# Optimization experiments

Measured on AMD Instinct MI355X. Metric: run time of the kernel, lower is better.

Reference implementation:

```python
import jax, jax.numpy as jnp
import numpy as np

K = 32        # neighbors kept
SCALE = 1     # dilation stride for dilated kNN


def setup_inputs() -> dict:
    key = jax.random.key(0)
    ks = jax.random.split(key, 8)
    s = 0.05  # weight init scale
    return {
        "x": jax.random.normal(ks[0], (16, 3, 4096), jnp.float32),
        "w1": jax.random.normal(ks[1], (64, 3), jnp.float32) * s,
        "b1": jnp.zeros((64,), jnp.float32),
        "w2": jax.random.normal(ks[2], (128, 64), jnp.float32) * s,
        "b2": jnp.zeros((128,), jnp.float32),
        "w3": jax.random.normal(ks[3], (1024, 128), jnp.float32) * s,
        "b3": jnp.zeros((1024,), jnp.float32),
        "fw1": jax.random.normal(ks[4], (512, 1024), jnp.float32) * s,
        "fb1": jnp.zeros((512,), jnp.float32),
        "fw2": jax.random.normal(ks[5], (256, 512), jnp.float32) * s,
        "fb2": jnp.zeros((256,), jnp.float32),
        "fw3": jax.random.normal(ks[6], (9, 256), jnp.float32) * s,
        "fb3": jnp.zeros((9,), jnp.float32),
    }


def _knn_idx(x):
    # x: (B, C, N). Returns (B, N, K) indices of K nearest neighbors (dilated by SCALE).
    inner = jnp.einsum('bcn,bcm->bnm', x, x)            # (B, N, N)
    sq = jnp.sum(x * x, axis=1)                          # (B, N)
    neg_dist = 2.0 * inner - sq[:, :, None] - sq[:, None, :]  # = -||xi-xj||^2
    _, idx = jax.lax.top_k(neg_dist, K * SCALE)          # (B, N, K*SCALE)
    return idx[:, :, ::SCALE]                            # (B, N, K)


def reference(x, w1, b1, w2, b2, w3, b3, fw1, fb1, fw2, fb2, fw3, fb3):
    B, C, N = x.shape
    idx = _knn_idx(x)                                    # (B, N, K)
    xt = jnp.swapaxes(x, 1, 2)                           # (B, N, C)
    # gather neighbors: nbrs[b,n,k,c] = xt[b, idx[b,n,k], c]
    nbrs = jax.vmap(lambda xb, ib: xb[ib])(xt, idx)      # (B, N, K, C)
    x0 = nbrs - xt[:, :, None, :]                        # edge features x_j - x_i

    # STN (T-Net): shared MLP over edges, global max pool, FC head -> 3x3 transform
    h = jax.nn.relu(jnp.einsum('bnkc,oc->bnko', x0, w1) + b1)
    h = jax.nn.relu(jnp.einsum('bnkc,oc->bnko', h, w2) + b2)
    h = jax.nn.relu(jnp.einsum('bnkc,oc->bnko', h, w3) + b3)
    g = jnp.max(h, axis=(1, 2))                          # (B, 1024)
    f = jax.nn.relu(g @ fw1.T + fb1)
    f = jax.nn.relu(f @ fw2.T + fb2)
    t = (f @ fw3.T + fb3).reshape(B, 3, 3) + jnp.eye(3, dtype=x.dtype)

    out = jnp.einsum('bnc,bcd->bnd', xt, t)              # bmm(x^T, t)
    return jnp.swapaxes(out, 1, 2)                       # (B, 3, N)
```

## Files before the change

kernel.cpp:

```cpp
#include <hip/hip_runtime.h>
#include <hip/hip_fp8.h>

typedef __bf16 bf16_t;
typedef __bf16 bf16x8 __attribute__((ext_vector_type(8)));
typedef float floatx16 __attribute__((ext_vector_type(16)));
typedef int intx8 __attribute__((ext_vector_type(8)));
typedef unsigned long long u64;

#define B_ 16
#define N_ 4096
#define K_ 32


__device__ __forceinline__ unsigned enc_f(float f) {
    unsigned u = __float_as_uint(f);
    return (u & 0x80000000u) ? ~u : (u | 0x80000000u);
}
__device__ __forceinline__ float dec_f(unsigned e) {
    return __uint_as_float((e & 0x80000000u) ? (e & 0x7fffffffu) : ~e);
}

__device__ __forceinline__ float max3f(float a, float b, float c) {
    float d;
    asm("v_max3_f32 %0, %1, %2, %3" : "=v"(d) : "v"(a), "v"(b), "v"(c));
    return d;
}

__device__ __forceinline__ void ce(unsigned& a, unsigned& b) {
    const unsigned mn = a < b ? a : b;
    const unsigned mx = a < b ? b : a;
    a = mn; b = mx;
}

__device__ __forceinline__ void sort8(unsigned* k) {
    ce(k[0], k[1]); ce(k[2], k[3]); ce(k[4], k[5]); ce(k[6], k[7]);
    ce(k[0], k[2]); ce(k[1], k[3]); ce(k[4], k[6]); ce(k[5], k[7]);
    ce(k[1], k[2]); ce(k[5], k[6]);
    ce(k[0], k[4]); ce(k[1], k[5]); ce(k[2], k[6]); ce(k[3], k[7]);
    ce(k[2], k[4]); ce(k[3], k[5]);
    ce(k[1], k[2]); ce(k[3], k[4]); ce(k[5], k[6]);
}
__device__ __forceinline__ void merge_top8(unsigned* r, const unsigned* k) {
    unsigned s[8];
    #pragma unroll
    for (int u = 0; u < 8; u++)
        s[u] = r[u] < k[7 - u] ? r[u] : k[7 - u];
    ce(s[0], s[4]); ce(s[1], s[5]); ce(s[2], s[6]); ce(s[3], s[7]);
    ce(s[0], s[2]); ce(s[1], s[3]); ce(s[4], s[6]); ce(s[5], s[7]);
    ce(s[0], s[1]); ce(s[2], s[3]); ce(s[4], s[5]); ce(s[6], s[7]);
    #pragma unroll
    for (int u = 0; u < 8; u++) r[u] = s[u];
}

__global__ __launch_bounds__(512, 4) void knn_kernel(
    const float* __restrict__ x, const float* __restrict__ w3,
    const float* __restrict__ w2, unsigned short* __restrict__ idxb,
    unsigned* __restrict__ g_enc, unsigned char* __restrict__ w3f8,
    bf16_t* __restrict__ w2sw)
{
    __shared__ __align__(16) float4 cand[16 * 257];
    unsigned* lists = (unsigned*)cand;
    unsigned* m1 = ((unsigned*)cand) + 8192;
    const int tid = threadIdx.x;
    const int bid = blockIdx.x;

    {
        const int g = bid * 512 + tid;
        if (g < 131072) {
            const int j  = g & 31;
            const int lI = (g >> 5) & 63;
            const int kq = (g >> 11) & 1;
            const int cb = g >> 12;
            const int mt2 = kq * 2 + (j >> 4), q = j & 15;
            const int lmI = lI & 31, hiI = lI >> 5;
            const int ch = mt2 * 32 + (q & 3) + 8 * (q >> 2) + 4 * hiI;
            __hip_fp8_e4m3 t(16.0f * w3[(cb * 32 + lmI) * 128 + ch]);
            w3f8[g] = t.__x;
        } else if (g < 139264) {
            const int o = g - 131072;
            const int f = o >> 9, r = o & 511, lI = r >> 3, jj = r & 7;
            const int ks = f & 3, nb = f >> 2, lmI = lI & 31, hiI = lI >> 5;
            const int ic = ks * 16 + 4 * hiI + 8 * (jj >> 2) + (jj & 3);
            w2sw[o] = (bf16_t)w2[(nb * 32 + lmI) * 64 + ic];
        } else if (g < 155648) {
            g_enc[g - 139264] = 0u;
        }
    }

    const int b  = bid >> 7;
    const int q  = tid >> 4;
    const int n  = (bid & 127) * 32 + q;
    const int t  = tid & 15;
    const float* xb = x + b * 3 * N_;

    for (int j = tid; j < N_; j += 512) {
        float cx = xb[j], cy = xb[N_ + j], cz = xb[2 * N_ + j];
        cand[j + (j >> 8)] = make_float4(-2.f * cx, -2.f * cy, -2.f * cz,
                                         fmaf(cx, cx, fmaf(cy, cy, cz * cz)));
    }
    __syncthreads();

    const float xi0 = xb[n], xi1 = xb[N_ + n], xi2 = xb[2 * N_ + n];
    const float xisq1 = fmaf(xi0, xi0, fmaf(xi1, xi1, xi2 * xi2)) + 1.0f;

    unsigned r[8];
    #pragma unroll
    for (int s = 0; s < 8; s++) r[s] = 0x7F7FFFFFu;

    const int j0 = t * 256;
    const int pb = t * 257;
    #pragma unroll 1
    for (int jb = 0; jb < 256; jb += 16) {
        unsigned ka[8], kb[8];
        #pragma unroll
        for (int u = 0; u < 8; u++) {
            const float4 c = cand[pb + jb + u];
            const float d = fmaf(c.z, xi2, fmaf(c.y, xi1, fmaf(c.x, xi0, c.w)));
            ka[u] = (__float_as_uint(d + xisq1) & 0xFFFFF000u)
                  | (unsigned)(j0 + jb + u);
        }
        #pragma unroll
        for (int u = 0; u < 8; u++) {
            const float4 c = cand[pb + jb + 8 + u];
            const float d = fmaf(c.z, xi2, fmaf(c.y, xi1, fmaf(c.x, xi0, c.w)));
            kb[u] = (__float_as_uint(d + xisq1) & 0xFFFFF000u)
                  | (unsigned)(j0 + jb + 8 + u);
        }
        sort8(ka);
        sort8(kb);
        merge_top8(ka, kb);
        merge_top8(r, ka);
    }
    __syncthreads();

    #pragma unroll
    for (int k = 0; k < 8; k++) lists[tid * 9 + k] = r[k];
    __syncthreads();

    if (tid < 128) {
        const int q1 = tid >> 2, gi = tid & 3;
        const int base = (q1 * 16 + gi * 4) * 9;
        unsigned h0 = lists[base], h1 = lists[base + 9];
        unsigned h2 = lists[base + 18], h3 = lists[base + 27];
        int p0 = 0, p1 = 0, p2 = 0, p3 = 0;
        unsigned* outp = m1 + (q1 * 4 + gi) * 32;
        #pragma unroll 1
        for (int k = 0; k < 32; k++) {
            const unsigned m01 = h0 < h1 ? h0 : h1;
            const unsigned m23 = h2 < h3 ? h2 : h3;
            const unsigned v = m01 < m23 ? m01 : m23;
            outp[k] = v;
            if (m01 < m23) {
                if (h1 < h0) { p1++; h1 = p1 < 8 ? lists[base + 9 + p1] : 0xFFFFFFFFu; }
                else         { p0++; h0 = p0 < 8 ? lists[base + p0]     : 0xFFFFFFFFu; }
            } else {
                if (h3 < h2) { p3++; h3 = p3 < 8 ? lists[base + 27 + p3] : 0xFFFFFFFFu; }
                else         { p2++; h2 = p2 < 8 ? lists[base + 18 + p2] : 0xFFFFFFFFu; }
            }
        }
    }
    __syncthreads();

    if (tid < 32) {
        const unsigned* g0 = m1 + tid * 128;
        unsigned h0 = g0[0], h1 = g0[32], h2 = g0[64], h3 = g0[96];
        int p0 = 0, p1 = 0, p2 = 0, p3 = 0;
        const int nq = (bid & 127) * 32 + tid;
        unsigned short* op = idxb + ((size_t)(b * N_ + nq)) * K_;
        #pragma unroll 1
        for (int k = 0; k < K_; k++) {
            const unsigned m01 = h0 < h1 ? h0 : h1;
            const unsigned m23 = h2 < h3 ? h2 : h3;
            const unsigned v = m01 < m23 ? m01 : m23;
            op[k] = (unsigned short)(v & 0xFFFu);
            if (m01 < m23) {
                if (h1 < h0) { p1++; h1 = p1 < 32 ? g0[32 + p1] : 0xFFFFFFFFu; }
                else         { p0++; h0 = p0 < 32 ? g0[p0]      : 0xFFFFFFFFu; }
            } else {
                if (h3 < h2) { p3++; h3 = p3 < 32 ? g0[96 + p3] : 0xFFFFFFFFu; }
                else         { p2++; h2 = p2 < 32 ? g0[64 + p2] : 0xFFFFFFFFu; }
            }
        }
    }
}

__device__ __forceinline__ void chunk_epilogue(
    const floatx16& a0, const floatx16& a1, int cb, unsigned* gl, int lm)
{
    float c0 = fmaxf(a0[0], a1[0]);
    float c1 = fmaxf(a0[1], a1[1]);
    float c2 = fmaxf(a0[2], a1[2]);
    float c3 = fmaxf(a0[3], a1[3]);
    #pragma unroll
    for (int o = 4; o < 16; o += 4) {
        c0 = max3f(a0[o + 0], a1[o + 0], c0);
        c1 = max3f(a0[o + 1], a1[o + 1], c1);
        c2 = max3f(a0[o + 2], a1[o + 2], c2);
        c3 = max3f(a0[o + 3], a1[o + 3], c3);
    }
    const float m = max3f(c0, c1, fmaxf(c2, c3));
    atomicMax(&gl[cb * 32 + lm], enc_f(m));
}

__global__ __launch_bounds__(256, 3) void mlp_kernel(
    const float* __restrict__ x, const unsigned short* __restrict__ idxb,
    const float* __restrict__ w1, const float* __restrict__ b1,
    const float* __restrict__ b2,
    const bf16_t* __restrict__ w2sw, const unsigned char* __restrict__ w3f8,
    unsigned* __restrict__ g_enc)
{
    __shared__ unsigned gl[1024];
    __shared__ __align__(16) float4 w1l[64];
    __shared__ __align__(16) float b2s[128];

    const int tid = threadIdx.x;
    const int b   = blockIdx.x >> 9;
    const int p0  = (blockIdx.x & 511) * 8;
    const float* xb = x + b * 3 * N_;

    const int wv = tid >> 6;
    const int l  = tid & 63;
    const int lm = l & 31;
    const int hi = l >> 5;

    for (int i = tid; i < 1024; i += 256) gl[i] = 0u;
    if (tid < 64)
        w1l[tid] = make_float4(w1[tid * 3], w1[tid * 3 + 1], w1[tid * 3 + 2], b1[tid]);
    else if (tid < 192)
        b2s[tid - 64] = 256.0f * b2[tid - 64];
    __syncthreads();

    const floatx16 zf = (floatx16)0.f;

    const unsigned char* w3p = w3f8 + l * 32;
#define PREFETCH_W3(dst, c) do {                                              \
        dst[0] = *(const intx8*)(w3p + (c) * 4096);                           \
        dst[1] = *(const intx8*)(w3p + (c) * 4096 + 2048);                    \
    } while (0)

    intx8 bwA[2], bwB[2];
    PREFETCH_W3(bwA, 0);

    float d0[2], d1[2], d2[2];
    #pragma unroll
    for (int nt2 = 0; nt2 < 2; nt2++) {
        const int pp = p0 + wv * 2 + nt2;
        const int j  = idxb[((size_t)(b * N_ + pp)) * K_ + lm];
        d0[nt2] = xb[j]          - xb[pp];
        d1[nt2] = xb[N_ + j]     - xb[N_ + pp];
        d2[nt2] = xb[2 * N_ + j] - xb[2 * N_ + pp];
    }

    bf16x8 a1f[2];
    #pragma unroll
    for (int tt = 0; tt < 2; tt++) {
        const float4 w = w1l[tt * 32 + lm];
        bf16x8 v = (bf16x8)(bf16_t)0.f;
        if (hi == 0) {
            v[0] = (bf16_t)w.x; v[1] = (bf16_t)w.y;
            v[2] = (bf16_t)w.z; v[3] = (bf16_t)w.w;
        }
        a1f[tt] = v;
    }

    bf16x8 b1h[2][4];
    #pragma unroll
    for (int nt2 = 0; nt2 < 2; nt2++) {
        bf16x8 bf = (bf16x8)(bf16_t)0.f;
        if (hi == 0) {
            bf[0] = (bf16_t)d0[nt2]; bf[1] = (bf16_t)d1[nt2];
            bf[2] = (bf16_t)d2[nt2]; bf[3] = (bf16_t)1.0f;
        }
        floatx16 hacc[2];
        hacc[0] = __builtin_amdgcn_mfma_f32_32x32x16_bf16(a1f[0], bf, zf, 0, 0, 0);
        hacc[1] = __builtin_amdgcn_mfma_f32_32x32x16_bf16(a1f[1], bf, zf, 0, 0, 0);
        #pragma unroll
        for (int ks = 0; ks < 4; ks++)
            #pragma unroll
            for (int jj = 0; jj < 8; jj++)
                b1h[nt2][ks][jj] = (bf16_t)fmaxf(
                    hacc[ks >> 1][(jj & 3) + 4 * (jj >> 2) + 8 * (ks & 1)], 0.f);
    }

    intx8 a3v[2][2];
    #pragma unroll
    for (int mt2 = 0; mt2 < 4; mt2++) {
        floatx16 acc0 = (floatx16)0.f, acc1 = (floatx16)0.f;
        #pragma unroll
        for (int ks = 0; ks < 4; ks++) {
            const bf16x8 aw = *(const bf16x8*)&w2sw[((mt2 * 4 + ks) * 64 + l) * 8];
            acc0 = __builtin_amdgcn_mfma_f32_32x32x16_bf16(aw, b1h[0][ks], acc0, 0, 0, 0);
            acc1 = __builtin_amdgcn_mfma_f32_32x32x16_bf16(aw, b1h[1][ks], acc1, 0, 0, 0);
        }
        const int kq = mt2 >> 1, c0 = (mt2 & 1) * 4;
        #pragma unroll
        for (int i2 = 0; i2 < 4; i2++) {
            const float4 bb = *(const float4*)&b2s[mt2 * 32 + i2 * 8 + hi * 4];
            {
                const float v0 = fmaxf(fmaf(acc0[4 * i2 + 0], 256.f, bb.x), 0.f);
                const float v1 = fmaxf(fmaf(acc0[4 * i2 + 1], 256.f, bb.y), 0.f);
                const float v2 = fmaxf(fmaf(acc0[4 * i2 + 2], 256.f, bb.z), 0.f);
                const float v3 = fmaxf(fmaf(acc0[4 * i2 + 3], 256.f, bb.w), 0.f);
                int w = __builtin_amdgcn_cvt_pk_fp8_f32(v0, v1, 0, false);
                w = __builtin_amdgcn_cvt_pk_fp8_f32(v2, v3, w, true);
                a3v[0][kq][c0 + i2] = w;
            }
            {
                const float v0 = fmaxf(fmaf(acc1[4 * i2 + 0], 256.f, bb.x), 0.f);
                const float v1 = fmaxf(fmaf(acc1[4 * i2 + 1], 256.f, bb.y), 0.f);
                const float v2 = fmaxf(fmaf(acc1[4 * i2 + 2], 256.f, bb.z), 0.f);
                const float v3 = fmaxf(fmaf(acc1[4 * i2 + 3], 256.f, bb.w), 0.f);
                int w = __builtin_amdgcn_cvt_pk_fp8_f32(v0, v1, 0, false);
                w = __builtin_amdgcn_cvt_pk_fp8_f32(v2, v3, w, true);
                a3v[1][kq][c0 + i2] = w;
            }
        }
    }

#define COMPUTE_W3(d0_, d1_, buf) do {                                        \
        __builtin_amdgcn_s_setprio(1);                                        \
        d0_ = __builtin_amdgcn_mfma_scale_f32_32x32x64_f8f6f4(                \
            a3v[0][0], buf[0], zf, 0, 0, 0, 0x7F7F7F7F, 0, 0x7F7F7F7F);       \
        d1_ = __builtin_amdgcn_mfma_scale_f32_32x32x64_f8f6f4(                \
            a3v[1][0], buf[0], zf, 0, 0, 0, 0x7F7F7F7F, 0, 0x7F7F7F7F);       \
        d0_ = __builtin_amdgcn_mfma_scale_f32_32x32x64_f8f6f4(                \
            a3v[0][1], buf[1], d0_, 0, 0, 0, 0x7F7F7F7F, 0, 0x7F7F7F7F);      \
        d1_ = __builtin_amdgcn_mfma_scale_f32_32x32x64_f8f6f4(                \
            a3v[1][1], buf[1], d1_, 0, 0, 0, 0x7F7F7F7F, 0, 0x7F7F7F7F);      \
        __builtin_amdgcn_s_setprio(0); } while (0)

    floatx16 pA0, pA1, pB0, pB1;

    PREFETCH_W3(bwB, 1);
    COMPUTE_W3(pA0, pA1, bwA);

    #pragma unroll 1
    for (int cc = 0; cc < 15; cc++) {
        PREFETCH_W3(bwA, 2 * cc + 2);
        COMPUTE_W3(pB0, pB1, bwB);
        chunk_epilogue(pA0, pA1, 2 * cc, gl, lm);
        PREFETCH_W3(bwB, 2 * cc + 3);
        COMPUTE_W3(pA0, pA1, bwA);
        chunk_epilogue(pB0, pB1, 2 * cc + 1, gl, lm);
    }
    COMPUTE_W3(pB0, pB1, bwB);
    chunk_epilogue(pA0, pA1, 30, gl, lm);
    chunk_epilogue(pB0, pB1, 31, gl, lm);

#undef PREFETCH_W3
#undef COMPUTE_W3

    __syncthreads();
    for (int i = tid; i < 1024; i += 256)
        atomicMax(&g_enc[b * 1024 + i], gl[i]);
}

__global__ __launch_bounds__(256) void head1_kernel(
    const unsigned* __restrict__ g_enc, const float* __restrict__ b3,
    const float* __restrict__ fw1, const float* __restrict__ fb1,
    float* __restrict__ f1buf)
{
    __shared__ __align__(16) float g[1024];
    __shared__ float red[256];
    const int t = threadIdx.x;
    const int b = blockIdx.x >> 3;
    const int s = blockIdx.x & 7;

    for (int i = t; i < 1024; i += 256)
        g[i] = fmaxf(fmaf(dec_f(g_enc[b * 1024 + i]), 2.44140625e-4f, b3[i]), 0.f);
    __syncthreads();

    const int o = s * 64 + (t & 63);
    const int quarter = t >> 6;
    const float4* wr = (const float4*)(fw1 + (size_t)o * 1024) + quarter * 64;
    const float4* gv = (const float4*)g + quarter * 64;
    float acc = 0.f;
    #pragma unroll 4
    for (int i = 0; i < 64; i++) {
        float4 a = wr[i], c = gv[i];
        acc = fmaf(a.x, c.x, acc); acc = fmaf(a.y, c.y, acc);
        acc = fmaf(a.z, c.z, acc); acc = fmaf(a.w, c.w, acc);
    }
    red[t] = acc;
    __syncthreads();
    if (t < 64) {
        const float v = red[t] + red[t + 64] + red[t + 128] + red[t + 192];
        f1buf[b * 512 + s * 64 + t] = fmaxf(v + fb1[s * 64 + t], 0.f);
    }
}

__global__ __launch_bounds__(256) void head2_kernel(
    const float* __restrict__ f1buf,
    const float* __restrict__ fw2, const float* __restrict__ fb2,
    const float* __restrict__ fw3, const float* __restrict__ fb3,
    float* __restrict__ tmat)
{
    __shared__ __align__(16) float f1[512];
    __shared__ __align__(16) float f2[256];
    const int t = threadIdx.x, b = blockIdx.x;

    if (t < 128) ((float4*)f1)[t] = ((const float4*)(f1buf + b * 512))[t];
    __syncthreads();
    {
        const int o = t;
        const float4* wr = (const float4*)(fw2 + (size_t)o * 512);
        const float4* fv = (const float4*)f1;
        float acc = fb2[o];
        for (int i = 0; i < 128; i++) {
            float4 a = wr[i], c = fv[i];
            acc = fmaf(a.x, c.x, acc); acc = fmaf(a.y, c.y, acc);
            acc = fmaf(a.z, c.z, acc); acc = fmaf(a.w, c.w, acc);
        }
        f2[o] = fmaxf(acc, 0.f);
    }
    __syncthreads();
    if (t < 9) {
        const float4* wr = (const float4*)(fw3 + (size_t)t * 256);
        const float4* fv = (const float4*)f2;
        float acc = fb3[t];
        for (int i = 0; i < 64; i++) {
            float4 a = wr[i], c = fv[i];
            acc = fmaf(a.x, c.x, acc); acc = fmaf(a.y, c.y, acc);
            acc = fmaf(a.z, c.z, acc); acc = fmaf(a.w, c.w, acc);
        }
        if (t == 0 || t == 4 || t == 8) acc += 1.f;
        tmat[b * 9 + t] = acc;
    }
}

__global__ __launch_bounds__(256) void out_kernel(
    const float* __restrict__ x, const float* __restrict__ tmat,
    float* __restrict__ out)
{
    const int gid = blockIdx.x * 256 + threadIdx.x;
    const int b = gid >> 12, n = gid & 4095;
    const float* T = tmat + b * 9;
    const float x0 = x[b * 12288 + n];
    const float x1 = x[b * 12288 + 4096 + n];
    const float x2 = x[b * 12288 + 8192 + n];
    #pragma unroll
    for (int d = 0; d < 3; d++)
        out[b * 12288 + d * 4096 + n] =
            fmaf(x2, T[6 + d], fmaf(x1, T[3 + d], x0 * T[d]));
}

extern "C" void kernel_launch(void* const* d_in, const int* in_sizes, int n_in,
                              void* d_out, int out_size, void* d_ws, size_t ws_size,
                              hipStream_t stream) {
    const float* x   = (const float*)d_in[0];
    const float* w1  = (const float*)d_in[1];
    const float* b1  = (const float*)d_in[2];
    const float* w2  = (const float*)d_in[3];
    const float* b2  = (const float*)d_in[4];
    const float* w3  = (const float*)d_in[5];
    const float* b3  = (const float*)d_in[6];
    const float* fw1 = (const float*)d_in[7];
    const float* fb1 = (const float*)d_in[8];
    const float* fw2 = (const float*)d_in[9];
    const float* fb2 = (const float*)d_in[10];
    const float* fw3 = (const float*)d_in[11];
    const float* fb3 = (const float*)d_in[12];
    float* out = (float*)d_out;

    char* ws = (char*)d_ws;
    unsigned short* idxb = (unsigned short*)ws;
    unsigned* g_enc = (unsigned*)(ws + 4194304);
    unsigned char* w3f8 = (unsigned char*)(ws + 4259840);
    bf16_t* w2sw = (bf16_t*)(ws + 4390912);
    float* tmat  = (float*)(ws + 4407296);
    float* f1buf = (float*)(ws + 4407872);

    knn_kernel<<<2048, 512, 0, stream>>>(x, w3, w2, idxb, g_enc, w3f8, w2sw);
    mlp_kernel<<<8192, 256, 0, stream>>>(x, idxb, w1, b1, b2, w2sw, w3f8, g_enc);
    head1_kernel<<<128, 256, 0, stream>>>(g_enc, b3, fw1, fb1, f1buf);
    head2_kernel<<<16, 256, 0, stream>>>(f1buf, fw2, fb2, fw3, fb3, tmat);
    out_kernel<<<256, 256, 0, stream>>>(x, tmat, out);
}
```

Measured before the change: 468.9 us.

## Stream kNN candidates in two LDS passes to halve shared memory and double occupancy

The kNN kernel now loads candidate points into LDS in two halves of 2048 instead of all 4096 at once, shrinking the shared buffer from about 66KB to about 35KB. Launch bounds are raised to 8 blocks per CU to use the freed LDS. The merge scratch is padded to a stride of 33 to avoid bank conflicts in the final 4-way merge. In exchange the kernel adds two extra block-wide barriers and reloads from global memory per pass, and the higher occupancy target may constrain registers.

```diff
diff --git a/kernel.cpp b/kernel.cpp
--- a/kernel.cpp
+++ b/kernel.cpp
@@ -52,15 +52,16 @@
     for (int u = 0; u < 8; u++) r[u] = s[u];
 }
 
-__global__ __launch_bounds__(512, 4) void knn_kernel(
+__global__ __launch_bounds__(512, 8) void knn_kernel(
     const float* __restrict__ x, const float* __restrict__ w3,
     const float* __restrict__ w2, unsigned short* __restrict__ idxb,
     unsigned* __restrict__ g_enc, unsigned char* __restrict__ w3f8,
     bf16_t* __restrict__ w2sw)
 {
-    __shared__ __align__(16) float4 cand[16 * 257];
-    unsigned* lists = (unsigned*)cand;
-    unsigned* m1 = ((unsigned*)cand) + 8192;
+    __shared__ __align__(16) unsigned smem_u[8832];
+    float4* cand = (float4*)smem_u;
+    unsigned* lists = smem_u;
+    unsigned* m1 = smem_u + 4608;
     const int tid = threadIdx.x;
     const int bid = blockIdx.x;
 
@@ -93,13 +94,6 @@
     const int t  = tid & 15;
     const float* xb = x + b * 3 * N_;
 
-    for (int j = tid; j < N_; j += 512) {
-        float cx = xb[j], cy = xb[N_ + j], cz = xb[2 * N_ + j];
-        cand[j + (j >> 8)] = make_float4(-2.f * cx, -2.f * cy, -2.f * cz,
-                                         fmaf(cx, cx, fmaf(cy, cy, cz * cz)));
-    }
-    __syncthreads();
-
     const float xi0 = xb[n], xi1 = xb[N_ + n], xi2 = xb[2 * N_ + n];
     const float xisq1 = fmaf(xi0, xi0, fmaf(xi1, xi1, xi2 * xi2)) + 1.0f;
 
@@ -107,29 +101,42 @@
     #pragma unroll
     for (int s = 0; s < 8; s++) r[s] = 0x7F7FFFFFu;
 
-    const int j0 = t * 256;
-    const int pb = t * 257;
+    const int pb = t * 128 + (t >> 1);
+
     #pragma unroll 1
-    for (int jb = 0; jb < 256; jb += 16) {
-        unsigned ka[8], kb[8];
-        #pragma unroll
-        for (int u = 0; u < 8; u++) {
-            const float4 c = cand[pb + jb + u];
-            const float d = fmaf(c.z, xi2, fmaf(c.y, xi1, fmaf(c.x, xi0, c.w)));
-            ka[u] = (__float_as_uint(d + xisq1) & 0xFFFFF000u)
-                  | (unsigned)(j0 + jb + u);
-        }
-        #pragma unroll
-        for (int u = 0; u < 8; u++) {
-            const float4 c = cand[pb + jb + 8 + u];
-            const float d = fmaf(c.z, xi2, fmaf(c.y, xi1, fmaf(c.x, xi0, c.w)));
-            kb[u] = (__float_as_uint(d + xisq1) & 0xFFFFF000u)
-                  | (unsigned)(j0 + jb + 8 + u);
-        }
-        sort8(ka);
-        sort8(kb);
-        merge_top8(ka, kb);
-        merge_top8(r, ka);
+    for (int pass = 0; pass < 2; pass++) {
+        __syncthreads();
+        for (int j = tid; j < 2048; j += 512) {
+            const int jg = pass * 2048 + j;
+            float cx = xb[jg], cy = xb[N_ + jg], cz = xb[2 * N_ + jg];
+            cand[j + (j >> 8)] = make_float4(-2.f * cx, -2.f * cy, -2.f * cz,
+                                             fmaf(cx, cx, fmaf(cy, cy, cz * cz)));
+        }
+        __syncthreads();
+
+        const int j0 = pass * 2048 + t * 128;
+        #pragma unroll 1
+        for (int jb = 0; jb < 128; jb += 16) {
+            unsigned ka[8], kb[8];
+            #pragma unroll
+            for (int u = 0; u < 8; u++) {
+                const float4 c = cand[pb + jb + u];
+                const float d = fmaf(c.z, xi2, fmaf(c.y, xi1, fmaf(c.x, xi0, c.w)));
+                ka[u] = (__float_as_uint(d + xisq1) & 0xFFFFF000u)
+                      | (unsigned)(j0 + jb + u);
+            }
+            #pragma unroll
+            for (int u = 0; u < 8; u++) {
+                const float4 c = cand[pb + jb + 8 + u];
+                const float d = fmaf(c.z, xi2, fmaf(c.y, xi1, fmaf(c.x, xi0, c.w)));
+                kb[u] = (__float_as_uint(d + xisq1) & 0xFFFFF000u)
+                      | (unsigned)(j0 + jb + 8 + u);
+            }
+            sort8(ka);
+            sort8(kb);
+            merge_top8(ka, kb);
+            merge_top8(r, ka);
+        }
     }
     __syncthreads();
 
@@ -143,7 +150,7 @@
         unsigned h0 = lists[base], h1 = lists[base + 9];
         unsigned h2 = lists[base + 18], h3 = lists[base + 27];
         int p0 = 0, p1 = 0, p2 = 0, p3 = 0;
-        unsigned* outp = m1 + (q1 * 4 + gi) * 32;
+        unsigned* outp = m1 + (q1 * 4 + gi) * 33;
         #pragma unroll 1
         for (int k = 0; k < 32; k++) {
             const unsigned m01 = h0 < h1 ? h0 : h1;
@@ -162,8 +169,11 @@
     __syncthreads();
 
     if (tid < 32) {
-        const unsigned* g0 = m1 + tid * 128;
-        unsigned h0 = g0[0], h1 = g0[32], h2 = g0[64], h3 = g0[96];
+        const unsigned* l0 = m1 + (tid * 4 + 0) * 33;
+        const unsigned* l1 = m1 + (tid * 4 + 1) * 33;
+        const unsigned* l2 = m1 + (tid * 4 + 2) * 33;
+        const unsigned* l3 = m1 + (tid * 4 + 3) * 33;
+        unsigned h0 = l0[0], h1 = l1[0], h2 = l2[0], h3 = l3[0];
         int p0 = 0, p1 = 0, p2 = 0, p3 = 0;
         const int nq = (bid & 127) * 32 + tid;
         unsigned short* op = idxb + ((size_t)(b * N_ + nq)) * K_;
@@ -174,11 +184,11 @@
             const unsigned v = m01 < m23 ? m01 : m23;
             op[k] = (unsigned short)(v & 0xFFFu);
             if (m01 < m23) {
-                if (h1 < h0) { p1++; h1 = p1 < 32 ? g0[32 + p1] : 0xFFFFFFFFu; }
-                else         { p0++; h0 = p0 < 32 ? g0[p0]      : 0xFFFFFFFFu; }
+                if (h1 < h0) { p1++; h1 = p1 < 32 ? l1[p1] : 0xFFFFFFFFu; }
+                else         { p0++; h0 = p0 < 32 ? l0[p0] : 0xFFFFFFFFu; }
             } else {
-                if (h3 < h2) { p3++; h3 = p3 < 32 ? g0[96 + p3] : 0xFFFFFFFFu; }
-                else         { p2++; h2 = p2 < 32 ? g0[64 + p2] : 0xFFFFFFFFu; }
+                if (h3 < h2) { p3++; h3 = p3 < 32 ? l3[p3] : 0xFFFFFFFFu; }
+                else         { p2++; h2 = p2 < 32 ? l2[p2] : 0xFFFFFFFFu; }
             }
         }
     }
```

Measured after the change: 454.8 us, median of 2. 3.0% less time.
